# Optimization experiments

Measured on AMD Instinct MI355X. Metric: run time of the kernel, lower is better.

## Reference

```python
import jax, jax.numpy as jnp
import numpy as np

B, N, NY = 2, 4096, 4096
ENC_DIM, DEC_DIM, H = 768, 512, 8
HEAD_DIM = DEC_DIM // H
SCALE = HEAD_DIM ** -0.5


def setup_inputs() -> dict:
    key = jax.random.key(0)
    ks = jax.random.split(key, 8)
    lim_q = 1.0 / np.sqrt(DEC_DIM)
    lim_kv = 1.0 / np.sqrt(ENC_DIM)
    return {
        "x": jax.random.normal(ks[0], (B, N, DEC_DIM), jnp.float32),
        "y": jax.random.normal(ks[1], (B, NY, ENC_DIM), jnp.float32),
        "key_padding_mask": jax.random.randint(ks[2], (B, NY), 0, 2).astype(bool),
        "Wq": jax.random.uniform(ks[3], (DEC_DIM, DEC_DIM), jnp.float32, -lim_q, lim_q),
        "Wkv": jax.random.uniform(ks[4], (2 * DEC_DIM, ENC_DIM), jnp.float32, -lim_kv, lim_kv),
        "Wp": jax.random.uniform(ks[5], (DEC_DIM, DEC_DIM), jnp.float32, -lim_q, lim_q),
        "bp": jax.random.uniform(ks[6], (DEC_DIM,), jnp.float32, -lim_q, lim_q),
    }


def reference(x, y, key_padding_mask, Wq, Wkv, Wp, bp):
    # q projection: [B,N,C] -> [B,H,N,D]
    q = (x @ Wq.T).reshape(B, N, H, HEAD_DIM).transpose(0, 2, 1, 3)
    # kv projection: [B,Ny,E] -> [B,Ny,2C] -> k,v each [B,H,Ny,D]
    kv = (y @ Wkv.T).reshape(B, NY, 2, H, HEAD_DIM).transpose(2, 0, 3, 1, 4)
    k, v = kv[0], kv[1]
    # attention scores [B,H,N,Ny]
    attn = jnp.einsum("bhnd,bhmd->bhnm", q, k) * SCALE
    attn = jnp.where(key_padding_mask[:, None, None, :], -jnp.inf, attn)
    attn = jax.nn.softmax(attn, axis=-1)
    out = jnp.einsum("bhnm,bhmd->bhnd", attn, v)  # [B,H,N,D]
    out = out.transpose(0, 2, 1, 3).reshape(B, N, DEC_DIM)
    return out @ Wp.T + bp
```

## Files before the change

### kernel.cpp

```cpp
#include <hip/hip_runtime.h>
#include <hip/hip_bf16.h>
#include <stdint.h>

typedef __bf16 bf16_t;
typedef __bf16 bf16x8 __attribute__((ext_vector_type(8)));
typedef __bf16 bf16x4 __attribute__((ext_vector_type(4)));
typedef float  f32x4  __attribute__((ext_vector_type(4)));

#define MFMA16(a, b, c) __builtin_amdgcn_mfma_f32_16x16x32_bf16((a), (b), (c), 0, 0, 0)

__device__ __forceinline__ void gload_lds16(const void* g, void* l) {
  __builtin_amdgcn_global_load_lds((const __attribute__((address_space(1))) void*)g,
                                   (__attribute__((address_space(3))) void*)l, 16, 0, 0);
}

#define QSCALE 0.18033688011112042f
#define NE_X   4194304UL
#define NE_Y   6291456UL
#define NE_WQ  262144UL
#define NE_WKV 786432UL
#define NE_WP  262144UL
#define NE_BP  512UL

__global__ void detect_and_mask(const uint16_t* __restrict__ xu,
                                const uint8_t* __restrict__ mk,
                                int* __restrict__ flags, bf16_t* __restrict__ mmul) {
  __shared__ int cbf, c3f1, c3f3, cnz;
  const int t = threadIdx.x;
  if (t == 0) { cbf = 0; c3f1 = 0; c3f3 = 0; cnz = 0; }
  __syncthreads();
  if (blockIdx.x == 0) {
    int local = 0;
    for (int i = t; i < 2048; i += 256) {
      uint16_t u = xu[2 * i];
      int e = (u >> 7) & 0xFF;
      if (u == 0 || (e >= 0x66 && e <= 0x88)) local++;
    }
    atomicAdd(&cbf, local);
  }
  int l1 = 0, l3 = 0, lnz = 0;
  for (int i = t; i < 4096; i += 256) {
    uint8_t b = mk[i];
    int p = i & 3;
    if (p == 1 && b == 0x3F) l1++;
    if (p == 3 && b == 0x3F) l3++;
    if (p != 0 && b != 0) lnz++;
  }
  atomicAdd(&c3f1, l1);
  atomicAdd(&c3f3, l3);
  atomicAdd(&cnz, lnz);
  __syncthreads();
  if (blockIdx.x == 0 && t == 0) flags[0] = (cbf > 1536) ? 1 : 0;
  const int fmt = (c3f1 > 0) ? 2 : (c3f3 > 0) ? 3 : (cnz > 0) ? 0 : 1;
  const int i = blockIdx.x * 256 + t;
  bool on;
  if (fmt == 0)      on = mk[i] != 0;
  else if (fmt == 1) on = ((const int*)mk)[i] != 0;
  else if (fmt == 2) on = (((const uint16_t*)mk)[i] & 0x7FFF) != 0;
  else               on = ((const float*)mk)[i] != 0.0f;
  mmul[i] = on ? (bf16_t)0.0f : (bf16_t)1.0f;
}

__global__ void convert_all(const void* __restrict__ x, const void* __restrict__ y,
                            const void* __restrict__ wq, const void* __restrict__ wkv,
                            const void* __restrict__ wp, const void* __restrict__ bp,
                            uint16_t* __restrict__ dst, const int* __restrict__ flags) {
  const size_t E0 = NE_X, E1 = E0 + NE_Y, E2 = E1 + NE_WQ, E3 = E2 + NE_WKV,
               E4 = E3 + NE_WP, E5 = E4 + NE_BP;
  size_t i8 = ((size_t)blockIdx.x * 256 + threadIdx.x) * 8;
  if (i8 >= E5) return;
  const void* src; size_t off;
  if      (i8 < E0) { src = x;   off = i8; }
  else if (i8 < E1) { src = y;   off = i8 - E0; }
  else if (i8 < E2) { src = wq;  off = i8 - E1; }
  else if (i8 < E3) { src = wkv; off = i8 - E2; }
  else if (i8 < E4) { src = wp;  off = i8 - E3; }
  else              { src = bp;  off = i8 - E4; }
  const bool isWq = (i8 >= E1 && i8 < E2);
  if (flags[0] && !isWq) {
    *(uint4*)(dst + i8) = *(const uint4*)((const uint16_t*)src + off);
    return;
  }
  float v[8];
  if (flags[0]) {
    const uint16_t* u = (const uint16_t*)src + off;
    for (int j = 0; j < 8; ++j) {
      union { uint32_t q; float f; } c; c.q = ((uint32_t)u[j]) << 16; v[j] = c.f;
    }
  } else {
    const float* f = (const float*)src + off;
    float4 a = *(const float4*)f;
    float4 b2 = *(const float4*)(f + 4);
    v[0] = a.x; v[1] = a.y; v[2] = a.z; v[3] = a.w;
    v[4] = b2.x; v[5] = b2.y; v[6] = b2.z; v[7] = b2.w;
  }
  const float sc = isWq ? QSCALE : 1.0f;
  union { bf16_t h[8]; uint4 u; } pk;
  for (int j = 0; j < 8; ++j) pk.h[j] = (bf16_t)(v[j] * sc);
  *(uint4*)(dst + i8) = pk.u;
}

template <int K, int MODE, int BN>
__device__ __forceinline__ void gemm_body(char* lds,
    const bf16_t* __restrict__ A, const bf16_t* __restrict__ W,
    const bf16_t* __restrict__ bias, void* __restrict__ C,
    bf16_t* __restrict__ Kf, bf16_t* __restrict__ Vf,
    const int* __restrict__ flags, int Ncols, int bx, int by) {
  constexpr int MT = (BN == 128) ? 4 : 2;
  char* ldsA = lds;
  char* ldsW = lds + 8192;
  const int t = threadIdx.x;
  const int w = t >> 6, lane = t & 63, quad = lane >> 4, l16 = lane & 15;
  const int wr = (BN == 128) ? (w >> 1) : w;
  const int wc = (BN == 128) ? (w & 1) : 0;
  const int m0 = by * 128, n0 = bx * BN;

  f32x4 acc[MT][4] = {};
  const int rowS = t >> 2, uS = t & 3;

  for (int k0 = 0; k0 < K; k0 += 32) {
    __syncthreads();
    for (int i = 0; i < 2; ++i) {
      int row = i * 64 + rowS;
      int c = uS ^ ((row >> 1) & 3);
      gload_lds16(A + (size_t)(m0 + row) * K + k0 + c * 8, ldsA + i * 4096 + w * 1024);
    }
    for (int i = 0; i < BN / 64; ++i) {
      int row = i * 64 + rowS;
      int c = uS ^ ((row >> 1) & 3);
      gload_lds16(W + (size_t)(n0 + row) * K + k0 + c * 8, ldsW + i * 4096 + w * 1024);
    }
    __syncthreads();
    bf16x8 af[MT], bfr[4];
    for (int mt = 0; mt < MT; ++mt) {
      int row = wr * (MT * 16) + mt * 16 + l16;
      int us = quad ^ ((row >> 1) & 3);
      af[mt] = *(const bf16x8*)(ldsA + row * 64 + us * 16);
    }
    for (int nt = 0; nt < 4; ++nt) {
      int row = wc * 64 + nt * 16 + l16;
      int us = quad ^ ((row >> 1) & 3);
      bfr[nt] = *(const bf16x8*)(ldsW + row * 64 + us * 16);
    }
    for (int mt = 0; mt < MT; ++mt)
      for (int nt = 0; nt < 4; ++nt)
        acc[mt][nt] = MFMA16(af[mt], bfr[nt], acc[mt][nt]);
  }

  const int mbase = m0 + wr * (MT * 16);
  for (int nt = 0; nt < 4; ++nt) {
    const int col = n0 + wc * 64 + nt * 16 + l16;
    if (MODE == 1 && col >= 512) {
      const int hd = col - 512;
      const int hh = hd >> 6, d = hd & 63;
      const int dt = d >> 4, l15 = d & 15;
      for (int mt = 0; mt < MT; ++mt) {
        int m = mbase + mt * 16 + quad * 4;
        int bb = m >> 12, keyg = m & 4095;
        int kt = keyg >> 6, keyin = keyg & 63;
        int kc = (keyin >> 5) & 1, jq = (keyin >> 3) & 3, j0 = keyin & 7;
        const bf16_t* mmp = bias + bb * 4096 + keyg;
        union { bf16_t h4[4]; uint2 u; } pk;
        for (int r = 0; r < 4; ++r) pk.h4[r] = (bf16_t)(acc[mt][nt][r] * (float)mmp[r]);
        size_t base = (((size_t)(bb * 8 + hh) * 64 + kt) * 8 + dt * 2 + kc) * 1024
                      + (jq * 16 + l15) * 16 + j0 * 2;
        *(uint2*)((char*)Vf + base) = pk.u;
      }
    } else if (MODE == 1) {
      const int hh = col >> 6, d = col & 63;
      const int kc = d >> 5, qd = (d >> 3) & 3, j = d & 7;
      for (int mt = 0; mt < MT; ++mt) {
        int m = mbase + mt * 16 + quad * 4;
        int bb = m >> 12, keyg = m & 4095;
        int kt = keyg >> 6, mtk = (keyg >> 4) & 3, l16k = keyg & 15;
        char* base = (char*)Kf + (((size_t)(bb * 8 + hh) * 64 + kt) * 8 + mtk * 2 + kc) * 1024
                     + (qd * 16 + l16k) * 16 + j * 2;
        for (int r = 0; r < 4; ++r)
          *(bf16_t*)(base + r * 16) = (bf16_t)acc[mt][nt][r];
      }
    } else if (MODE == 0) {
      for (int mt = 0; mt < MT; ++mt) {
        int m = mbase + mt * 16 + quad * 4;
        for (int r = 0; r < 4; ++r)
          ((bf16_t*)C)[(size_t)(m + r) * Ncols + col] = (bf16_t)acc[mt][nt][r];
      }
    } else {
      const float bv = (float)bias[col];
      const bool obf = (flags[0] != 0);
      for (int mt = 0; mt < MT; ++mt) {
        int m = mbase + mt * 16 + quad * 4;
        for (int r = 0; r < 4; ++r) {
          float v = acc[mt][nt][r] + bv;
          if (obf) ((bf16_t*)C)[(size_t)(m + r) * Ncols + col] = (bf16_t)v;
          else     ((float*)C)[(size_t)(m + r) * Ncols + col] = v;
        }
      }
    }
  }
}

__launch_bounds__(256, 2)
__global__ void proj_kv(const bf16_t* __restrict__ Yb, const bf16_t* __restrict__ Wkvb,
                        const bf16_t* __restrict__ mmul, bf16_t* __restrict__ Kfr,
                        bf16_t* __restrict__ Vfr) {
  __shared__ __align__(16) char lds[16384];
  gemm_body<768, 1, 128>(lds, Yb, Wkvb, mmul, nullptr, Kfr, Vfr, nullptr, 1024,
                         blockIdx.x, blockIdx.y);
}

__launch_bounds__(256, 2)
__global__ void proj_q(const bf16_t* __restrict__ Xb, const bf16_t* __restrict__ Wqb,
                       bf16_t* __restrict__ Qbuf) {
  __shared__ __align__(16) char lds[12288];
  gemm_body<512, 0, 64>(lds, Xb, Wqb, nullptr, Qbuf, nullptr, nullptr, nullptr, 512,
                        blockIdx.x, blockIdx.y);
}

__launch_bounds__(256, 2)
__global__ void gemm_out(const bf16_t* __restrict__ Obuf, const bf16_t* __restrict__ Wpb,
                         const bf16_t* __restrict__ bpb, void* __restrict__ out,
                         const int* __restrict__ flags) {
  __shared__ __align__(16) char lds[12288];
  gemm_body<512, 2, 64>(lds, Obuf, Wpb, bpb, out, nullptr, nullptr, flags, 512,
                        blockIdx.x, blockIdx.y);
}

__launch_bounds__(256, 2)
__global__ void attn(const bf16_t* __restrict__ Qb, const bf16_t* __restrict__ Kfb,
                     const bf16_t* __restrict__ Vfb, const bf16_t* __restrict__ mmul,
                     bf16_t* __restrict__ Ob) {
  const int t = threadIdx.x, w = t >> 6, lane = t & 63, quad = lane >> 4, l16 = lane & 15;
  const int h = blockIdx.y, b = blockIdx.z;
  const int qw0 = blockIdx.x * 128 + w * 32;

  __shared__ __align__(16) char lds[16384];
  char* Pw = lds + w * 4096;

  bf16x8 qf[2][2];
  for (int ng = 0; ng < 2; ++ng)
    for (int kc = 0; kc < 2; ++kc)
      qf[ng][kc] = *(const bf16x8*)(Qb + (size_t)(b * 4096 + qw0 + ng * 16 + l16) * 512
                                    + h * 64 + kc * 32 + quad * 8);

  const char* Kfbase = (const char*)Kfb + (size_t)(b * 8 + h) * 524288;
  const char* Vfbase = (const char*)Vfb + (size_t)(b * 8 + h) * 524288;
  const bf16_t* mbase_p = mmul + b * 4096;

  f32x4 o[2][4] = {};
  f32x4 lacc[2] = {};
  bf16x8 kf0[8], kf1[8];

  {
    const char* Kt = Kfbase;
    for (int i = 0; i < 8; ++i) kf0[i] = *(const bf16x8*)(Kt + i * 1024 + lane * 16);
  }

  auto do_tile = [&](const bf16x8 (&kfb)[8], bf16x8 (&kfn)[8], int kt, bool pref) {
    const char* Vt = Vfbase + (size_t)kt * 8192;
    bf16x8 vf[8];
    for (int i = 0; i < 8; ++i) vf[i] = *(const bf16x8*)(Vt + i * 1024 + lane * 16);
    bf16x8 mfa = *(const bf16x8*)(mbase_p + kt * 64 + quad * 8);
    bf16x8 mfb = *(const bf16x8*)(mbase_p + kt * 64 + 32 + quad * 8);
    if (pref) {
      const char* Kn = Kfbase + (size_t)(kt + 1) * 8192;
      for (int i = 0; i < 8; ++i) kfn[i] = *(const bf16x8*)(Kn + i * 1024 + lane * 16);
    }
    for (int ng = 0; ng < 2; ++ng) {
      const int row = ng * 16 + l16;
      for (int mt = 0; mt < 4; ++mt) {
        f32x4 z = {};
        z = MFMA16(kfb[mt * 2 + 0], qf[ng][0], z);
        z = MFMA16(kfb[mt * 2 + 1], qf[ng][1], z);
        bf16x4 pk;
        pk.x = (bf16_t)__builtin_amdgcn_exp2f(z[0]);
        pk.y = (bf16_t)__builtin_amdgcn_exp2f(z[1]);
        pk.z = (bf16_t)__builtin_amdgcn_exp2f(z[2]);
        pk.w = (bf16_t)__builtin_amdgcn_exp2f(z[3]);
        int c2 = (2 * mt + (quad >> 1)) ^ (row & 7);
        *(bf16x4*)(Pw + row * 128 + c2 * 16 + (quad & 1) * 8) = pk;
      }
    }
    bf16x8 pf[2][2];
    for (int ng = 0; ng < 2; ++ng)
      for (int kc = 0; kc < 2; ++kc) {
        int row = ng * 16 + l16;
        int u = (4 * kc + quad) ^ (row & 7);
        pf[ng][kc] = *(const bf16x8*)(Pw + row * 128 + u * 16);
      }
    lacc[0] = MFMA16(pf[0][0], mfa, lacc[0]);
    lacc[0] = MFMA16(pf[0][1], mfb, lacc[0]);
    lacc[1] = MFMA16(pf[1][0], mfa, lacc[1]);
    lacc[1] = MFMA16(pf[1][1], mfb, lacc[1]);
    for (int dt = 0; dt < 4; ++dt)
      for (int kc = 0; kc < 2; ++kc) {
        o[0][dt] = MFMA16(pf[0][kc], vf[dt * 2 + kc], o[0][dt]);
        o[1][dt] = MFMA16(pf[1][kc], vf[dt * 2 + kc], o[1][dt]);
      }
  };

  for (int kt = 0; kt < 64; kt += 2) {
    do_tile(kf0, kf1, kt, true);
    do_tile(kf1, kf0, kt + 1, kt + 2 < 64);
  }

  for (int ng = 0; ng < 2; ++ng) {
    float inv[4];
    for (int r = 0; r < 4; ++r) inv[r] = 1.0f / lacc[ng][r];
    for (int dt = 0; dt < 4; ++dt)
      for (int r = 0; r < 4; ++r) {
        int q = qw0 + ng * 16 + quad * 4 + r;
        int col = h * 64 + dt * 16 + l16;
        Ob[(size_t)(b * 4096 + q) * 512 + col] = (bf16_t)(o[ng][dt][r] * inv[r]);
      }
  }
}

extern "C" void kernel_launch(void* const* d_in, const int* in_sizes, int n_in,
                              void* d_out, int out_size, void* d_ws, size_t ws_size,
                              hipStream_t stream) {
  const void* x   = d_in[0];
  const void* y   = d_in[1];
  const void* msk = d_in[2];
  const void* Wq  = d_in[3];
  const void* Wkv = d_in[4];
  const void* Wp  = d_in[5];
  const void* bp  = d_in[6];

  char* ws = (char*)d_ws;
  bf16_t* Xb   = (bf16_t*)(ws + 0);
  bf16_t* Yb   = (bf16_t*)(ws + 8388608);
  bf16_t* Wqb  = (bf16_t*)(ws + 20971520);
  bf16_t* Wkvb = (bf16_t*)(ws + 21495808);
  bf16_t* Wpb  = (bf16_t*)(ws + 23068672);
  bf16_t* bpb  = (bf16_t*)(ws + 23592960);
  bf16_t* mmul = (bf16_t*)(ws + 23593984);
  int*    flags = (int*)(ws + 23610368);
  bf16_t* Kfrag = (bf16_t*)(ws + 25165824);
  bf16_t* Vfrag = (bf16_t*)(ws + 33554432);
  bf16_t* Qbuf  = (bf16_t*)(ws + 8388608);
  bf16_t* Obuf  = (bf16_t*)(ws + 0);

  hipLaunchKernelGGL(detect_and_mask, dim3(32), dim3(256), 0, stream,
                     (const uint16_t*)x, (const uint8_t*)msk, flags, mmul);
  hipLaunchKernelGGL(convert_all, dim3(5761), dim3(256), 0, stream,
                     x, y, Wq, Wkv, Wp, bp, (uint16_t*)ws, flags);
  hipLaunchKernelGGL(proj_kv, dim3(8, 64), dim3(256), 0, stream,
                     Yb, Wkvb, mmul, Kfrag, Vfrag);
  hipLaunchKernelGGL(proj_q, dim3(8, 64), dim3(256), 0, stream,
                     Xb, Wqb, Qbuf);
  hipLaunchKernelGGL(attn, dim3(32, 8, 2), dim3(256), 0, stream,
                     Qbuf, Kfrag, Vfrag, mmul, Obuf);
  hipLaunchKernelGGL(gemm_out, dim3(8, 64), dim3(256), 0, stream,
                     Obuf, Wpb, bpb, d_out, flags);
}
```

Measured before the change: 282.2 us.

## Merge Q and KV projections into one launch and shrink attention tiles

Merges the Q and KV projection GEMMs into a single launch using a z-dimension switch. When the workspace is large enough, Q is written to a separate buffer so it no longer aliases Yb. The attention kernel now handles 16 query rows per wave instead of 32, with a bh-major grid, half the LDS and launch bounds raised to 4 blocks per SM. A per-tile barrier is added to keep waves sharing K/V in lockstep. Together these aim for more occupancy and better L2 reuse of K/V, at the cost of each K/V fragment serving half as many queries and extra barrier overhead.

Result: slower. 305.6 us (+8.3%).

```diff
diff --git a/kernel.cpp b/kernel.cpp
--- a/kernel.cpp
+++ b/kernel.cpp
@@ -217,6 +217,20 @@
 }
 
 __launch_bounds__(256, 2)
+__global__ void proj_all(const bf16_t* __restrict__ Yb, const bf16_t* __restrict__ Wkvb,
+                         const bf16_t* __restrict__ mmul, bf16_t* __restrict__ Kfr,
+                         bf16_t* __restrict__ Vfr, const bf16_t* __restrict__ Xb,
+                         const bf16_t* __restrict__ Wqb, bf16_t* __restrict__ Qbuf) {
+  __shared__ __align__(16) char lds[16384];
+  if (blockIdx.z == 0)
+    gemm_body<768, 1, 128>(lds, Yb, Wkvb, mmul, nullptr, Kfr, Vfr, nullptr, 1024,
+                           blockIdx.x, blockIdx.y);
+  else
+    gemm_body<512, 0, 64>(lds, Xb, Wqb, nullptr, Qbuf, nullptr, nullptr, nullptr, 512,
+                          blockIdx.x, blockIdx.y);
+}
+
+__launch_bounds__(256, 2)
 __global__ void gemm_out(const bf16_t* __restrict__ Obuf, const bf16_t* __restrict__ Wpb,
                          const bf16_t* __restrict__ bpb, void* __restrict__ out,
                          const int* __restrict__ flags) {
@@ -225,37 +239,34 @@
                         blockIdx.x, blockIdx.y);
 }
 
-__launch_bounds__(256, 2)
+__launch_bounds__(256, 4)
 __global__ void attn(const bf16_t* __restrict__ Qb, const bf16_t* __restrict__ Kfb,
                      const bf16_t* __restrict__ Vfb, const bf16_t* __restrict__ mmul,
                      bf16_t* __restrict__ Ob) {
   const int t = threadIdx.x, w = t >> 6, lane = t & 63, quad = lane >> 4, l16 = lane & 15;
-  const int h = blockIdx.y, b = blockIdx.z;
-  const int qw0 = blockIdx.x * 128 + w * 32;
-
-  __shared__ __align__(16) char lds[16384];
-  char* Pw = lds + w * 4096;
-
-  bf16x8 qf[2][2];
-  for (int ng = 0; ng < 2; ++ng)
-    for (int kc = 0; kc < 2; ++kc)
-      qf[ng][kc] = *(const bf16x8*)(Qb + (size_t)(b * 4096 + qw0 + ng * 16 + l16) * 512
-                                    + h * 64 + kc * 32 + quad * 8);
-
-  const char* Kfbase = (const char*)Kfb + (size_t)(b * 8 + h) * 524288;
-  const char* Vfbase = (const char*)Vfb + (size_t)(b * 8 + h) * 524288;
+  const int bh = blockIdx.x, b = bh >> 3, h = bh & 7;
+  const int qw0 = blockIdx.y * 64 + w * 16;
+
+  __shared__ __align__(16) char lds[8192];
+  char* Pw = lds + w * 2048;
+
+  bf16x8 qf[2];
+  for (int kc = 0; kc < 2; ++kc)
+    qf[kc] = *(const bf16x8*)(Qb + (size_t)(b * 4096 + qw0 + l16) * 512
+                              + h * 64 + kc * 32 + quad * 8);
+
+  const char* Kfbase = (const char*)Kfb + (size_t)bh * 524288;
+  const char* Vfbase = (const char*)Vfb + (size_t)bh * 524288;
   const bf16_t* mbase_p = mmul + b * 4096;
 
-  f32x4 o[2][4] = {};
-  f32x4 lacc[2] = {};
+  f32x4 o[4] = {};
+  f32x4 lacc = {};
   bf16x8 kf0[8], kf1[8];
 
-  {
-    const char* Kt = Kfbase;
-    for (int i = 0; i < 8; ++i) kf0[i] = *(const bf16x8*)(Kt + i * 1024 + lane * 16);
-  }
+  for (int i = 0; i < 8; ++i) kf0[i] = *(const bf16x8*)(Kfbase + i * 1024 + lane * 16);
 
   auto do_tile = [&](const bf16x8 (&kfb)[8], bf16x8 (&kfn)[8], int kt, bool pref) {
+    __builtin_amdgcn_s_barrier();
     const char* Vt = Vfbase + (size_t)kt * 8192;
     bf16x8 vf[8];
     for (int i = 0; i < 8; ++i) vf[i] = *(const bf16x8*)(Vt + i * 1024 + lane * 16);
@@ -265,37 +276,30 @@
       const char* Kn = Kfbase + (size_t)(kt + 1) * 8192;
       for (int i = 0; i < 8; ++i) kfn[i] = *(const bf16x8*)(Kn + i * 1024 + lane * 16);
     }
-    for (int ng = 0; ng < 2; ++ng) {
-      const int row = ng * 16 + l16;
-      for (int mt = 0; mt < 4; ++mt) {
-        f32x4 z = {};
-        z = MFMA16(kfb[mt * 2 + 0], qf[ng][0], z);
-        z = MFMA16(kfb[mt * 2 + 1], qf[ng][1], z);
-        bf16x4 pk;
-        pk.x = (bf16_t)__builtin_amdgcn_exp2f(z[0]);
-        pk.y = (bf16_t)__builtin_amdgcn_exp2f(z[1]);
-        pk.z = (bf16_t)__builtin_amdgcn_exp2f(z[2]);
-        pk.w = (bf16_t)__builtin_amdgcn_exp2f(z[3]);
-        int c2 = (2 * mt + (quad >> 1)) ^ (row & 7);
-        *(bf16x4*)(Pw + row * 128 + c2 * 16 + (quad & 1) * 8) = pk;
-      }
-    }
-    bf16x8 pf[2][2];
-    for (int ng = 0; ng < 2; ++ng)
-      for (int kc = 0; kc < 2; ++kc) {
-        int row = ng * 16 + l16;
-        int u = (4 * kc + quad) ^ (row & 7);
-        pf[ng][kc] = *(const bf16x8*)(Pw + row * 128 + u * 16);
-      }
-    lacc[0] = MFMA16(pf[0][0], mfa, lacc[0]);
-    lacc[0] = MFMA16(pf[0][1], mfb, lacc[0]);
-    lacc[1] = MFMA16(pf[1][0], mfa, lacc[1]);
-    lacc[1] = MFMA16(pf[1][1], mfb, lacc[1]);
-    for (int dt = 0; dt < 4; ++dt)
-      for (int kc = 0; kc < 2; ++kc) {
-        o[0][dt] = MFMA16(pf[0][kc], vf[dt * 2 + kc], o[0][dt]);
-        o[1][dt] = MFMA16(pf[1][kc], vf[dt * 2 + kc], o[1][dt]);
-      }
+    const int row = l16;
+    for (int mt = 0; mt < 4; ++mt) {
+      f32x4 z = {};
+      z = MFMA16(kfb[mt * 2 + 0], qf[0], z);
+      z = MFMA16(kfb[mt * 2 + 1], qf[1], z);
+      bf16x4 pk;
+      pk.x = (bf16_t)__builtin_amdgcn_exp2f(z[0]);
+      pk.y = (bf16_t)__builtin_amdgcn_exp2f(z[1]);
+      pk.z = (bf16_t)__builtin_amdgcn_exp2f(z[2]);
+      pk.w = (bf16_t)__builtin_amdgcn_exp2f(z[3]);
+      int c2 = (2 * mt + (quad >> 1)) ^ (row & 7);
+      *(bf16x4*)(Pw + row * 128 + c2 * 16 + (quad & 1) * 8) = pk;
+    }
+    bf16x8 pf[2];
+    for (int kc = 0; kc < 2; ++kc) {
+      int u = (4 * kc + quad) ^ (row & 7);
+      pf[kc] = *(const bf16x8*)(Pw + row * 128 + u * 16);
+    }
+    lacc = MFMA16(pf[0], mfa, lacc);
+    lacc = MFMA16(pf[1], mfb, lacc);
+    for (int dt = 0; dt < 4; ++dt) {
+      o[dt] = MFMA16(pf[0], vf[dt * 2 + 0], o[dt]);
+      o[dt] = MFMA16(pf[1], vf[dt * 2 + 1], o[dt]);
+    }
   };
 
   for (int kt = 0; kt < 64; kt += 2) {
@@ -303,16 +307,14 @@
     do_tile(kf1, kf0, kt + 1, kt + 2 < 64);
   }
 
-  for (int ng = 0; ng < 2; ++ng) {
-    float inv[4];
-    for (int r = 0; r < 4; ++r) inv[r] = 1.0f / lacc[ng][r];
-    for (int dt = 0; dt < 4; ++dt)
-      for (int r = 0; r < 4; ++r) {
-        int q = qw0 + ng * 16 + quad * 4 + r;
-        int col = h * 64 + dt * 16 + l16;
-        Ob[(size_t)(b * 4096 + q) * 512 + col] = (bf16_t)(o[ng][dt][r] * inv[r]);
-      }
-  }
+  float inv[4];
+  for (int r = 0; r < 4; ++r) inv[r] = 1.0f / lacc[r];
+  for (int dt = 0; dt < 4; ++dt)
+    for (int r = 0; r < 4; ++r) {
+      int q = qw0 + quad * 4 + r;
+      int col = h * 64 + dt * 16 + l16;
+      Ob[(size_t)(b * 4096 + q) * 512 + col] = (bf16_t)(o[dt][r] * inv[r]);
+    }
 }
 
 extern "C" void kernel_launch(void* const* d_in, const int* in_sizes, int n_in,
@@ -337,18 +339,26 @@
   int*    flags = (int*)(ws + 23610368);
   bf16_t* Kfrag = (bf16_t*)(ws + 25165824);
   bf16_t* Vfrag = (bf16_t*)(ws + 33554432);
-  bf16_t* Qbuf  = (bf16_t*)(ws + 8388608);
   bf16_t* Obuf  = (bf16_t*)(ws + 0);
+
+  const bool big = (ws_size >= 50331648);
+  bf16_t* Qbuf = big ? (bf16_t*)(ws + 41943040)
+                     : (bf16_t*)(ws + 8388608);
 
   hipLaunchKernelGGL(detect_and_mask, dim3(32), dim3(256), 0, stream,
                      (const uint16_t*)x, (const uint8_t*)msk, flags, mmul);
   hipLaunchKernelGGL(convert_all, dim3(5761), dim3(256), 0, stream,
                      x, y, Wq, Wkv, Wp, bp, (uint16_t*)ws, flags);
-  hipLaunchKernelGGL(proj_kv, dim3(8, 64), dim3(256), 0, stream,
-                     Yb, Wkvb, mmul, Kfrag, Vfrag);
-  hipLaunchKernelGGL(proj_q, dim3(8, 64), dim3(256), 0, stream,
-                     Xb, Wqb, Qbuf);
-  hipLaunchKernelGGL(attn, dim3(32, 8, 2), dim3(256), 0, stream,
+  if (big) {
+    hipLaunchKernelGGL(proj_all, dim3(8, 64, 2), dim3(256), 0, stream,
+                       Yb, Wkvb, mmul, Kfrag, Vfrag, Xb, Wqb, Qbuf);
+  } else {
+    hipLaunchKernelGGL(proj_kv, dim3(8, 64), dim3(256), 0, stream,
+                       Yb, Wkvb, mmul, Kfrag, Vfrag);
+    hipLaunchKernelGGL(proj_q, dim3(8, 64), dim3(256), 0, stream,
+                       Xb, Wqb, Qbuf);
+  }
+  hipLaunchKernelGGL(attn, dim3(16, 64), dim3(256), 0, stream,
                      Qbuf, Kfrag, Vfrag, mmul, Obuf);
   hipLaunchKernelGGL(gemm_out, dim3(8, 64), dim3(256), 0, stream,
                      Obuf, Wpb, bpb, d_out, flags);
```
